# Kernel tuning notes

Hardware: AMD Instinct MI355X
Metric: run time of the kernel (lower is better)

The kernel has to match this reference:

```python
import jax, jax.numpy as jnp
import numpy as np

DIM = 128
B = 262144


def setup_inputs() -> dict:
    key = jax.random.key(0)
    k_t, k_w1, k_b1, k_w2, k_b2 = jax.random.split(key, 5)
    t = jax.random.uniform(k_t, (B,), dtype=jnp.float32)  # t in [0, 1]
    s = 1.0 / np.sqrt(DIM)  # torch Linear default init scale
    W1 = jax.random.uniform(k_w1, (DIM, DIM), dtype=jnp.float32, minval=-s, maxval=s)
    b1 = jax.random.uniform(k_b1, (DIM,), dtype=jnp.float32, minval=-s, maxval=s)
    W2 = jax.random.uniform(k_w2, (DIM, DIM), dtype=jnp.float32, minval=-s, maxval=s)
    b2 = jax.random.uniform(k_b2, (DIM,), dtype=jnp.float32, minval=-s, maxval=s)
    return {"t": t, "W1": W1, "b1": b1, "W2": W2, "b2": b2}


def reference(t, W1, b1, W2, b2):
    # create_timestep_embedding, vectorized over batch and dim:
    #   emb[b, i] = t[b]*cos(i/dim*pi*t[b]) + t[b]*sin(i/dim*pi*(1 - t[b]))
    phase = (jnp.arange(DIM, dtype=t.dtype) / DIM) * jnp.pi  # [DIM]
    tb = t[:, None]  # [B, 1]
    emb = tb * jnp.cos(phase[None, :] * tb) + tb * jnp.sin(phase[None, :] * (1.0 - tb))  # [B, DIM]
    x = jax.nn.silu(emb @ W1.T + b1)  # Linear128 + SiLU
    x = jax.nn.silu(x @ W2.T + b2)    # Linear128 + SiLU
    return x
```

## Files before the change

kernel.cpp:

```cpp
#include <hip/hip_runtime.h>

typedef _Float16 f16;
typedef _Float16 f16x2 __attribute__((ext_vector_type(2)));
typedef _Float16 f16x8 __attribute__((ext_vector_type(8)));
typedef float    f32x4 __attribute__((ext_vector_type(4)));

#define DIM 128

__device__ __forceinline__ float silu_f(float x) {
    float e = __builtin_amdgcn_exp2f(x * -1.44269504088896341f);
    return x * __builtin_amdgcn_rcpf(1.0f + e);
}

__global__ __launch_bounds__(1024, 4)
void ts_mlp_kernel(const float* __restrict__ t,
                   const float* __restrict__ W1, const float* __restrict__ b1,
                   const float* __restrict__ W2, const float* __restrict__ b2,
                   float* __restrict__ out, int B) {
    __shared__ f16x8 w1f[4][8][64];
    __shared__ f16x8 w2f[4][8][64];
    __shared__ f16x2 x1p[16][256][4];

    const int tid  = threadIdx.x;
    const int wv   = tid >> 6;
    const int lane = tid & 63;
    const int q    = lane >> 4;
    const int ln   = lane & 15;
    const int par  = lane & 1;

    {
        const int mtx = wv >> 3;
        const int nt  = wv & 7;
        const float* W = mtx ? W2 : W1;
        const int n = nt * 16 + ln;
#pragma unroll
        for (int kt = 0; kt < 4; ++kt) {
            const int k0 = kt * 32 + q * 8;
            const float4* src = (const float4*)(W + n * DIM + k0);
            float4 lo = src[0], hi = src[1];
            f16x8 fr;
            fr[0] = (f16)lo.x; fr[1] = (f16)lo.y; fr[2] = (f16)lo.z; fr[3] = (f16)lo.w;
            fr[4] = (f16)hi.x; fr[5] = (f16)hi.y; fr[6] = (f16)hi.z; fr[7] = (f16)hi.w;
            if (mtx) w2f[kt][nt][lane] = fr; else w1f[kt][nt][lane] = fr;
        }
    }
    float b1v[8], b2v[8];
#pragma unroll
    for (int nt = 0; nt < 8; ++nt) {
        b1v[nt] = b1[nt * 16 + ln];
        b2v[nt] = b2[nt * 16 + ln];
    }
    __syncthreads();

    const int ntiles = B >> 8;
    int tile = blockIdx.x;
    float tv_next = (tile < ntiles) ? t[tile * 256 + wv * 16 + ln] : 0.0f;

    for (; tile < ntiles; tile += gridDim.x) {
        const float tv = tv_next;
        const int nxt = tile + gridDim.x;
        if (nxt < ntiles) tv_next = t[nxt * 256 + wv * 16 + ln];
        const int row0 = tile * 256 + wv * 16;

        const float t256 = tv * 0.00390625f;
        const float o256 = (1.0f - tv) * 0.00390625f;
        f16x8 af[4];
#pragma unroll
        for (int kt = 0; kt < 4; ++kt) {
#pragma unroll
            for (int j = 0; j < 8; ++j) {
                const float fd = (float)(kt * 32 + q * 8 + j);
                const float c  = __builtin_amdgcn_cosf(fd * t256);
                const float s  = __builtin_amdgcn_sinf(fd * o256);
                af[kt][j] = (f16)(tv * (c + s));
            }
        }

        f32x4 acc[8];
#pragma unroll
        for (int nt = 0; nt < 8; ++nt) acc[nt] = (f32x4){0.f, 0.f, 0.f, 0.f};
#pragma unroll
        for (int kt = 0; kt < 4; ++kt) {
#pragma unroll
            for (int nt = 0; nt < 8; ++nt) {
                acc[nt] = __builtin_amdgcn_mfma_f32_16x16x32_f16(
                    af[kt], w1f[kt][nt][lane], acc[nt], 0, 0, 0);
            }
        }

#pragma unroll
        for (int nt = 0; nt < 8; ++nt) {
            float v[4], pv[4];
#pragma unroll
            for (int r = 0; r < 4; ++r) v[r] = silu_f(acc[nt][r] + b1v[nt]);
#pragma unroll
            for (int r = 0; r < 4; ++r) pv[r] = __shfl_xor(v[r], 1, 64);
            const int k0  = nt * 16 + (ln & 14);
            const int cch = k0 >> 3;
            const int hw  = (k0 & 7) >> 1;
#pragma unroll
            for (int p = 0; p < 2; ++p) {
                const int r = par * 2 + p;
                const int m = q * 4 + r;
                const float lo = par ? pv[r] : v[r];
                const float hi = par ? v[r] : pv[r];
                f16x2 h; h.x = (f16)lo; h.y = (f16)hi;
                x1p[wv][m * 16 + (cch ^ m)][hw] = h;
            }
        }

        f32x4 acc2[8];
#pragma unroll
        for (int nt = 0; nt < 8; ++nt) acc2[nt] = (f32x4){0.f, 0.f, 0.f, 0.f};
#pragma unroll
        for (int kt = 0; kt < 4; ++kt) {
            const f16x8 a2 = *(const f16x8*)&x1p[wv][ln * 16 + ((kt * 4 + q) ^ ln)][0];
#pragma unroll
            for (int nt = 0; nt < 8; ++nt) {
                acc2[nt] = __builtin_amdgcn_mfma_f32_16x16x32_f16(
                    a2, w2f[kt][nt][lane], acc2[nt], 0, 0, 0);
            }
        }

#pragma unroll
        for (int nt = 0; nt < 8; ++nt) {
#pragma unroll
            for (int r = 0; r < 4; ++r) {
                const float o = silu_f(acc2[nt][r] + b2v[nt]);
                out[(size_t)(row0 + q * 4 + r) * DIM + nt * 16 + ln] = o;
            }
        }
    }
}

extern "C" void kernel_launch(void* const* d_in, const int* in_sizes, int n_in,
                              void* d_out, int out_size, void* d_ws, size_t ws_size,
                              hipStream_t stream) {
    const float* t  = (const float*)d_in[0];
    const float* W1 = (const float*)d_in[1];
    const float* b1 = (const float*)d_in[2];
    const float* W2 = (const float*)d_in[3];
    const float* b2 = (const float*)d_in[4];
    float* out = (float*)d_out;
    const int B = in_sizes[0];
    const int ntiles = B >> 8;
    int grid = ntiles < 256 ? ntiles : 256;
    ts_mlp_kernel<<<dim3(grid), dim3(1024), 0, stream>>>(t, W1, b1, W2, b2, out, B);
}
```

Measured before the change: 196.4 us.

## Switch both MLP layers to 32x32x16 MFMA with 32-row wave tiles

Replaces the 16x16x32 f16 MFMA with the 32x32x16 variant, so each wave processes 32 rows instead of 16 and the block shrinks to 512 threads (8 waves). The weight fragment layout in LDS, the swizzled intermediate buffer and the output indexing are reworked for the 32x32 accumulator layout. The intent is fewer MFMA instructions, better operand reuse per instruction and less per-row overhead. In exchange each thread holds 64 accumulator floats per layer, which raises register pressure and the launch bound is lowered to 512 threads with 2 blocks per CU.

```diff
diff --git a/kernel.cpp b/kernel.cpp
--- a/kernel.cpp
+++ b/kernel.cpp
@@ -3,7 +3,7 @@
 typedef _Float16 f16;
 typedef _Float16 f16x2 __attribute__((ext_vector_type(2)));
 typedef _Float16 f16x8 __attribute__((ext_vector_type(8)));
-typedef float    f32x4 __attribute__((ext_vector_type(4)));
+typedef float    f32x16 __attribute__((ext_vector_type(16)));
 
 #define DIM 128
 
@@ -12,122 +12,129 @@
     return x * __builtin_amdgcn_rcpf(1.0f + e);
 }
 
-__global__ __launch_bounds__(1024, 4)
+__global__ __launch_bounds__(512, 2)
 void ts_mlp_kernel(const float* __restrict__ t,
                    const float* __restrict__ W1, const float* __restrict__ b1,
                    const float* __restrict__ W2, const float* __restrict__ b2,
                    float* __restrict__ out, int B) {
-    __shared__ f16x8 w1f[4][8][64];
-    __shared__ f16x8 w2f[4][8][64];
-    __shared__ f16x2 x1p[16][256][4];
+    __shared__ f16x8 w1f[8][4][64];
+    __shared__ f16x8 w2f[8][4][64];
+    __shared__ f16x2 x1p[8][512][4];
 
     const int tid  = threadIdx.x;
     const int wv   = tid >> 6;
     const int lane = tid & 63;
-    const int q    = lane >> 4;
-    const int ln   = lane & 15;
+    const int h    = lane >> 5;
+    const int l31  = lane & 31;
     const int par  = lane & 1;
 
     {
-        const int mtx = wv >> 3;
-        const int nt  = wv & 7;
-        const float* W = mtx ? W2 : W1;
-        const int n = nt * 16 + ln;
+        const int kt = wv;
+        const int k0 = kt * 16 + h * 8;
 #pragma unroll
-        for (int kt = 0; kt < 4; ++kt) {
-            const int k0 = kt * 32 + q * 8;
-            const float4* src = (const float4*)(W + n * DIM + k0);
-            float4 lo = src[0], hi = src[1];
-            f16x8 fr;
-            fr[0] = (f16)lo.x; fr[1] = (f16)lo.y; fr[2] = (f16)lo.z; fr[3] = (f16)lo.w;
-            fr[4] = (f16)hi.x; fr[5] = (f16)hi.y; fr[6] = (f16)hi.z; fr[7] = (f16)hi.w;
-            if (mtx) w2f[kt][nt][lane] = fr; else w1f[kt][nt][lane] = fr;
+        for (int mtx = 0; mtx < 2; ++mtx) {
+            const float* W = mtx ? W2 : W1;
+#pragma unroll
+            for (int nt = 0; nt < 4; ++nt) {
+                const int n = nt * 32 + l31;
+                const float4* src = (const float4*)(W + n * DIM + k0);
+                float4 lo = src[0], hi = src[1];
+                f16x8 fr;
+                fr[0] = (f16)lo.x; fr[1] = (f16)lo.y; fr[2] = (f16)lo.z; fr[3] = (f16)lo.w;
+                fr[4] = (f16)hi.x; fr[5] = (f16)hi.y; fr[6] = (f16)hi.z; fr[7] = (f16)hi.w;
+                if (mtx) w2f[kt][nt][lane] = fr; else w1f[kt][nt][lane] = fr;
+            }
         }
     }
-    float b1v[8], b2v[8];
+    float b1v[4], b2v[4];
 #pragma unroll
-    for (int nt = 0; nt < 8; ++nt) {
-        b1v[nt] = b1[nt * 16 + ln];
-        b2v[nt] = b2[nt * 16 + ln];
+    for (int nt = 0; nt < 4; ++nt) {
+        b1v[nt] = b1[nt * 32 + l31];
+        b2v[nt] = b2[nt * 32 + l31];
     }
     __syncthreads();
 
     const int ntiles = B >> 8;
     int tile = blockIdx.x;
-    float tv_next = (tile < ntiles) ? t[tile * 256 + wv * 16 + ln] : 0.0f;
+    float tv_next = (tile < ntiles) ? t[tile * 256 + wv * 32 + l31] : 0.0f;
+    const float h8f = (float)(h * 8);
 
     for (; tile < ntiles; tile += gridDim.x) {
         const float tv = tv_next;
         const int nxt = tile + gridDim.x;
-        if (nxt < ntiles) tv_next = t[nxt * 256 + wv * 16 + ln];
-        const int row0 = tile * 256 + wv * 16;
+        if (nxt < ntiles) tv_next = t[nxt * 256 + wv * 32 + l31];
+        const int row0 = tile * 256 + wv * 32;
 
         const float t256 = tv * 0.00390625f;
         const float o256 = (1.0f - tv) * 0.00390625f;
-        f16x8 af[4];
+        f16x8 af[8];
 #pragma unroll
-        for (int kt = 0; kt < 4; ++kt) {
+        for (int kt = 0; kt < 8; ++kt) {
 #pragma unroll
             for (int j = 0; j < 8; ++j) {
-                const float fd = (float)(kt * 32 + q * 8 + j);
+                const float fd = (float)(kt * 16 + j) + h8f;
                 const float c  = __builtin_amdgcn_cosf(fd * t256);
                 const float s  = __builtin_amdgcn_sinf(fd * o256);
                 af[kt][j] = (f16)(tv * (c + s));
             }
         }
 
-        f32x4 acc[8];
+        f32x16 acc[4];
 #pragma unroll
-        for (int nt = 0; nt < 8; ++nt) acc[nt] = (f32x4){0.f, 0.f, 0.f, 0.f};
+        for (int nt = 0; nt < 4; ++nt)
 #pragma unroll
-        for (int kt = 0; kt < 4; ++kt) {
+            for (int r = 0; r < 16; ++r) acc[nt][r] = 0.0f;
 #pragma unroll
-            for (int nt = 0; nt < 8; ++nt) {
-                acc[nt] = __builtin_amdgcn_mfma_f32_16x16x32_f16(
+        for (int kt = 0; kt < 8; ++kt) {
+#pragma unroll
+            for (int nt = 0; nt < 4; ++nt) {
+                acc[nt] = __builtin_amdgcn_mfma_f32_32x32x16_f16(
                     af[kt], w1f[kt][nt][lane], acc[nt], 0, 0, 0);
             }
         }
 
 #pragma unroll
-        for (int nt = 0; nt < 8; ++nt) {
-            float v[4], pv[4];
+        for (int nt = 0; nt < 4; ++nt) {
+            float v[16], pv[16];
 #pragma unroll
-            for (int r = 0; r < 4; ++r) v[r] = silu_f(acc[nt][r] + b1v[nt]);
+            for (int r = 0; r < 16; ++r) v[r] = silu_f(acc[nt][r] + b1v[nt]);
 #pragma unroll
-            for (int r = 0; r < 4; ++r) pv[r] = __shfl_xor(v[r], 1, 64);
-            const int k0  = nt * 16 + (ln & 14);
-            const int cch = k0 >> 3;
-            const int hw  = (k0 & 7) >> 1;
+            for (int r = 0; r < 16; ++r) pv[r] = __shfl_xor(v[r], 1, 64);
+            const int cch = nt * 4 + ((lane & 30) >> 3);
+            const int dw  = (lane & 6) >> 1;
 #pragma unroll
-            for (int p = 0; p < 2; ++p) {
-                const int r = par * 2 + p;
-                const int m = q * 4 + r;
+            for (int w8 = 0; w8 < 8; ++w8) {
+                const int r   = par * 8 + w8;
+                const int row = (r & 3) + 8 * (r >> 2) + 4 * h;
                 const float lo = par ? pv[r] : v[r];
                 const float hi = par ? v[r] : pv[r];
-                f16x2 h; h.x = (f16)lo; h.y = (f16)hi;
-                x1p[wv][m * 16 + (cch ^ m)][hw] = h;
+                f16x2 hh; hh.x = (f16)lo; hh.y = (f16)hi;
+                x1p[wv][row * 16 + (cch ^ (row & 15))][dw] = hh;
             }
         }
 
-        f32x4 acc2[8];
+        f32x16 acc2[4];
 #pragma unroll
-        for (int nt = 0; nt < 8; ++nt) acc2[nt] = (f32x4){0.f, 0.f, 0.f, 0.f};
+        for (int nt = 0; nt < 4; ++nt)
 #pragma unroll
-        for (int kt = 0; kt < 4; ++kt) {
-            const f16x8 a2 = *(const f16x8*)&x1p[wv][ln * 16 + ((kt * 4 + q) ^ ln)][0];
+            for (int r = 0; r < 16; ++r) acc2[nt][r] = 0.0f;
 #pragma unroll
-            for (int nt = 0; nt < 8; ++nt) {
-                acc2[nt] = __builtin_amdgcn_mfma_f32_16x16x32_f16(
+        for (int kt = 0; kt < 8; ++kt) {
+            const f16x8 a2 = *(const f16x8*)&x1p[wv][l31 * 16 + ((kt * 2 + h) ^ (l31 & 15))][0];
+#pragma unroll
+            for (int nt = 0; nt < 4; ++nt) {
+                acc2[nt] = __builtin_amdgcn_mfma_f32_32x32x16_f16(
                     a2, w2f[kt][nt][lane], acc2[nt], 0, 0, 0);
             }
         }
 
 #pragma unroll
-        for (int nt = 0; nt < 8; ++nt) {
+        for (int nt = 0; nt < 4; ++nt) {
 #pragma unroll
-            for (int r = 0; r < 4; ++r) {
+            for (int r = 0; r < 16; ++r) {
+                const int row = (r & 3) + 8 * (r >> 2) + 4 * h;
                 const float o = silu_f(acc2[nt][r] + b2v[nt]);
-                out[(size_t)(row0 + q * 4 + r) * DIM + nt * 16 + ln] = o;
+                out[(size_t)(row0 + row) * DIM + nt * 32 + l31] = o;
             }
         }
     }
@@ -145,5 +152,5 @@
     const int B = in_sizes[0];
     const int ntiles = B >> 8;
     int grid = ntiles < 256 ? ntiles : 256;
-    ts_mlp_kernel<<<dim3(grid), dim3(1024), 0, stream>>>(t, W1, b1, W2, b2, out, B);
+    ts_mlp_kernel<<<dim3(grid), dim3(512), 0, stream>>>(t, W1, b1, W2, b2, out, B);
 }
```

After: 194.6 us. No clear change (-0.9%).
